# Performance work log

Hardware: AMD Instinct MI355X
Metric: run time of the kernel (lower is better)

Reference implementation:

```python
import jax, jax.numpy as jnp
import numpy as np

B, T1, T2, D = 4, 128, 128, 300


def setup_inputs() -> dict:
    key = jax.random.key(0)
    ks = jax.random.split(key, 9)
    s = 1.0 / np.sqrt(D)
    return {
        "query": jax.random.normal(ks[0], (B, T1, D), jnp.float32),
        "key": jax.random.normal(ks[1], (B, T2, D), jnp.float32),
        "value": jax.random.normal(ks[2], (B, T2, D), jnp.float32),
        "hL": jax.random.normal(ks[3], (B, T1, T2, D), jnp.float32),
        "hR": jax.random.normal(ks[4], (B, T2, T1, D), jnp.float32),
        "WQ": jax.random.uniform(ks[5], (D, D), jnp.float32, -s, s),
        "bQ": jax.random.uniform(ks[6], (D,), jnp.float32, -s, s),
        "WK": jax.random.uniform(ks[7], (D, D), jnp.float32, -s, s),
        "bK": jax.random.uniform(ks[8], (D,), jnp.float32, -s, s),
    }


def reference(query, key, value, hL, hR, WQ, bQ, WK, bK):
    # Linear projections (torch nn.Linear: x @ W.T + b). Note fwK is applied
    # to BOTH key and value in the original module.
    q = query @ WQ.T + bQ            # [B, T1, D]
    k = key @ WK.T + bK              # [B, T2, D]
    v = value @ WK.T + bK            # [B, T2, D]

    hR_t = jnp.swapaxes(hR, 1, 2)    # [B, T1, T2, D]

    # concept-augmented scores: (q_i + hL_ij) . (k_j + hR_ji)
    q_plus_hL = q[:, :, None, :] + hL          # [B, T1, T2, D]
    k_plus_hR = k[:, None, :, :] + hR_t        # [B, T1, T2, D]
    scores = jnp.einsum("bijd,bijd->bij", q_plus_hL, k_plus_hR)  # [B, T1, T2]

    p_attn = jax.nn.softmax(scores, axis=-1)   # [B, T1, T2] (dropout p=0.0)

    # sharpening=True path: re-softmax with temperature 1/1000 then clamp
    attn = jnp.clip(jax.nn.softmax(1000.0 * p_attn, axis=-1), 0.0, 1.0)

    v_aug = v[:, None, :, :] + hR_t            # [B, T1, T2, D]
    x = jnp.einsum("bij,bijd->bid", attn, v_aug)  # [B, T1, D]
    return x
```

## Files before the change

kernel.cpp:

```cpp
#include <hip/hip_runtime.h>

#define BB 4
#define T 128
#define D 300
#define D4 75
#define NROW 512

__global__ __launch_bounds__(320) void proj_kernel(
    const float* __restrict__ query, const float* __restrict__ key,
    const float* __restrict__ value,
    const float* __restrict__ WQ, const float* __restrict__ bQ,
    const float* __restrict__ WK, const float* __restrict__ bK,
    float* __restrict__ qkv )
{
    const int src  = blockIdx.x >> 6;
    const int rblk = blockIdx.x & 63;
    const int r0   = rblk * 8;
    const float* in   = (src == 0) ? query : (src == 1 ? key : value);
    const float* W    = (src == 0) ? WQ : WK;
    const float* bias = (src == 0) ? bQ : bK;
    float* out = qkv + src * (NROW * D);

    __shared__ __align__(16) float lds_in[8 * D];
    for (int idx = threadIdx.x; idx < 8 * D; idx += 320)
        lds_in[idx] = in[r0 * D + idx];
    __syncthreads();

    const int t = threadIdx.x;
    if (t < D) {
        float acc[8];
        const float bv = bias[t];
        #pragma unroll
        for (int r = 0; r < 8; ++r) acc[r] = bv;
        const float4* W4 = (const float4*)(W + t * D);
        for (int e4 = 0; e4 < D4; ++e4) {
            const float4 w = W4[e4];
            #pragma unroll
            for (int r = 0; r < 8; ++r) {
                const float4 x = *(const float4*)(&lds_in[r * D + e4 * 4]);
                acc[r] += w.x * x.x + w.y * x.y + w.z * x.z + w.w * x.w;
            }
        }
        #pragma unroll
        for (int r = 0; r < 8; ++r)
            out[(r0 + r) * D + t] = acc[r];
    }
}

__global__ __launch_bounds__(1024) void attn_kernel(
    const float* __restrict__ hL, const float* __restrict__ hR,
    const float* __restrict__ qkv, float* __restrict__ outp)
{
    const int b = blockIdx.x >> 7;
    const int i = blockIdx.x & 127;

    const float* qp    = qkv + (b * T + i) * D;
    const float* kbase = qkv + NROW * D + b * T * D;
    const float* vbase = qkv + 2 * NROW * D + b * T * D;

    __shared__ __align__(16) float q_lds[D];
    __shared__ float sc[T];
    __shared__ __align__(16) float red[12][D];

    for (int idx = threadIdx.x; idx < D; idx += 1024) q_lds[idx] = qp[idx];
    __syncthreads();

    const int wave = threadIdx.x >> 6;
    const int lane = threadIdx.x & 63;

    const float4* hL4 = (const float4*)(hL + (size_t)(b * T + i) * T * D);
    for (int j = wave; j < T; j += 16) {
        const float4* hRrow = (const float4*)(hR + ((size_t)(b * T + j) * T + i) * D);
        const float4* krow  = (const float4*)(kbase + j * D);
        float4 a = {0.f, 0.f, 0.f, 0.f};
        #pragma unroll
        for (int it = 0; it < 2; ++it) {
            const int d4 = lane + it * 64;
            if (d4 < D4) {
                const float4 l  = hL4[j * D4 + d4];
                const float4 r  = hRrow[d4];
                const float4 kk = krow[d4];
                const float4 qq = *(const float4*)(&q_lds[d4 * 4]);
                a.x += (qq.x + l.x) * (kk.x + r.x);
                a.y += (qq.y + l.y) * (kk.y + r.y);
                a.z += (qq.z + l.z) * (kk.z + r.z);
                a.w += (qq.w + l.w) * (kk.w + r.w);
            }
        }
        float s = a.x + a.y + a.z + a.w;
        #pragma unroll
        for (int off = 32; off > 0; off >>= 1)
            s += __shfl_down(s, off, 64);
        if (lane == 0) sc[j] = s;
    }
    __syncthreads();

    if (wave == 0) {
        float s0 = sc[lane], s1 = sc[lane + 64];
        float m = fmaxf(s0, s1);
        #pragma unroll
        for (int off = 32; off > 0; off >>= 1) m = fmaxf(m, __shfl_xor(m, off, 64));
        float e0 = __expf(s0 - m), e1 = __expf(s1 - m);
        float sum = e0 + e1;
        #pragma unroll
        for (int off = 32; off > 0; off >>= 1) sum += __shfl_xor(sum, off, 64);
        const float inv = 1.0f / sum;
        float t0 = 1000.0f * (e0 * inv), t1 = 1000.0f * (e1 * inv);
        float m2 = fmaxf(t0, t1);
        #pragma unroll
        for (int off = 32; off > 0; off >>= 1) m2 = fmaxf(m2, __shfl_xor(m2, off, 64));
        float f0 = __expf(t0 - m2), f1 = __expf(t1 - m2);
        float sum2 = f0 + f1;
        #pragma unroll
        for (int off = 32; off > 0; off >>= 1) sum2 += __shfl_xor(sum2, off, 64);
        const float inv2 = 1.0f / sum2;
        sc[lane]      = fminf(fmaxf(f0 * inv2, 0.f), 1.f);
        sc[lane + 64] = fminf(fmaxf(f1 * inv2, 0.f), 1.f);
    }
    __syncthreads();

    const int tid = threadIdx.x;
    if (tid < 12 * D4) {
        const int grp = tid / D4;
        const int d4  = tid % D4;
        float4 acc = {0.f, 0.f, 0.f, 0.f};
        for (int j = grp; j < T; j += 12) {
            const float aj = sc[j];
            if (aj >= 1e-12f) {
                const float4 v4 = *(const float4*)(vbase + j * D + d4 * 4);
                const float4 r4 = *(const float4*)(hR + ((size_t)(b * T + j) * T + i) * D + d4 * 4);
                acc.x += aj * (v4.x + r4.x);
                acc.y += aj * (v4.y + r4.y);
                acc.z += aj * (v4.z + r4.z);
                acc.w += aj * (v4.w + r4.w);
            }
        }
        *(float4*)(&red[grp][d4 * 4]) = acc;
    }
    __syncthreads();
    if (tid < D4) {
        float4 o = {0.f, 0.f, 0.f, 0.f};
        #pragma unroll
        for (int g = 0; g < 12; ++g) {
            const float4 p = *(const float4*)(&red[g][tid * 4]);
            o.x += p.x; o.y += p.y; o.z += p.z; o.w += p.w;
        }
        *(float4*)(outp + (size_t)(b * T + i) * D + tid * 4) = o;
    }
}

extern "C" void kernel_launch(void* const* d_in, const int* in_sizes, int n_in,
                              void* d_out, int out_size, void* d_ws, size_t ws_size,
                              hipStream_t stream) {
    const float* query = (const float*)d_in[0];
    const float* key   = (const float*)d_in[1];
    const float* value = (const float*)d_in[2];
    const float* hL    = (const float*)d_in[3];
    const float* hR    = (const float*)d_in[4];
    const float* WQ    = (const float*)d_in[5];
    const float* bQ    = (const float*)d_in[6];
    const float* WK    = (const float*)d_in[7];
    const float* bK    = (const float*)d_in[8];
    float* out = (float*)d_out;
    float* qkv = (float*)d_ws;

    proj_kernel<<<dim3(192), dim3(320), 0, stream>>>(query, key, value, WQ, bQ, WK, bK, qkv);
    attn_kernel<<<dim3(512), dim3(1024), 0, stream>>>(hL, hR, qkv, out);
}
```

Before: 227.4 us.

## Split attention into tiled score kernel and separate softmax/output kernel

Replaces the per-query-row attention kernel with a score kernel that processes 4x4 (i,j) tiles. Each tile stages contiguous 4-row runs of hL and hR into shared memory, so hR is read as contiguous chunks instead of one strided row per j. Scores go to a workspace buffer. A second kernel applies the double softmax and the weighted sum over v+hR with scalar loads per d. This adds a kernel launch and a round-trip of the scores through global memory, and hR is still read again with strides in the output phase.

```diff
diff --git a/kernel.cpp b/kernel.cpp
--- a/kernel.cpp
+++ b/kernel.cpp
@@ -47,56 +47,79 @@
     }
 }
 
-__global__ __launch_bounds__(1024) void attn_kernel(
+__global__ __launch_bounds__(256) void score_kernel(
     const float* __restrict__ hL, const float* __restrict__ hR,
-    const float* __restrict__ qkv, float* __restrict__ outp)
+    const float* __restrict__ qkv, float* __restrict__ S)
+{
+    const int b  = blockIdx.x >> 10;
+    const int it = (blockIdx.x >> 5) & 31;
+    const int jt = blockIdx.x & 31;
+    const int i0 = it * 4, j0 = jt * 4;
+
+    __shared__ __align__(16) float4 lds[2400];
+
+    const float4* hL4 = (const float4*)hL;
+    const float4* hR4 = (const float4*)hR;
+
+    for (int f = threadIdx.x; f < 2400; f += 256) {
+        if (f < 1200) {
+            const int run = f / 300;
+            const int t   = f - run * 300;
+            lds[f] = hL4[(size_t)((b * T + i0 + run) * T + j0) * D4 + t];
+        } else {
+            const int g   = f - 1200;
+            const int run = g / 300;
+            const int t   = g - run * 300;
+            lds[f] = hR4[(size_t)((b * T + j0 + run) * T + i0) * D4 + t];
+        }
+    }
+    __syncthreads();
+
+    const int w    = threadIdx.x >> 6;
+    const int lane = threadIdx.x & 63;
+
+    const float4* q4     = (const float4*)(qkv) + (size_t)(b * T + i0 + w) * D4;
+    const float4* kbase4 = (const float4*)(qkv + NROW * D);
+
+    const float4 qa = q4[lane];
+    float4 qb = {0.f, 0.f, 0.f, 0.f};
+    if (lane < D4 - 64) qb = q4[64 + lane];
+
+    #pragma unroll
+    for (int jl = 0; jl < 4; ++jl) {
+        const float4* k4 = kbase4 + (size_t)(b * T + j0 + jl) * D4;
+        const float4 ka = k4[lane];
+        const float4 la = lds[w * 300 + jl * 75 + lane];
+        const float4 ra = lds[1200 + jl * 300 + w * 75 + lane];
+        float s = (qa.x + la.x) * (ka.x + ra.x) + (qa.y + la.y) * (ka.y + ra.y)
+                + (qa.z + la.z) * (ka.z + ra.z) + (qa.w + la.w) * (ka.w + ra.w);
+        if (lane < D4 - 64) {
+            const float4 kb = k4[64 + lane];
+            const float4 lb = lds[w * 300 + jl * 75 + 64 + lane];
+            const float4 rb = lds[1200 + jl * 300 + w * 75 + 64 + lane];
+            s += (qb.x + lb.x) * (kb.x + rb.x) + (qb.y + lb.y) * (kb.y + rb.y)
+               + (qb.z + lb.z) * (kb.z + rb.z) + (qb.w + lb.w) * (kb.w + rb.w);
+        }
+        #pragma unroll
+        for (int off = 32; off > 0; off >>= 1)
+            s += __shfl_down(s, off, 64);
+        if (lane == 0)
+            S[(size_t)(b * T + i0 + w) * T + j0 + jl] = s;
+    }
+}
+
+__global__ __launch_bounds__(320) void out_kernel(
+    const float* __restrict__ S, const float* __restrict__ qkv,
+    const float* __restrict__ hR, float* __restrict__ outp)
 {
     const int b = blockIdx.x >> 7;
     const int i = blockIdx.x & 127;
+    __shared__ float sc[T];
+    const int tid = threadIdx.x;
 
-    const float* qp    = qkv + (b * T + i) * D;
-    const float* kbase = qkv + NROW * D + b * T * D;
-    const float* vbase = qkv + 2 * NROW * D + b * T * D;
-
-    __shared__ __align__(16) float q_lds[D];
-    __shared__ float sc[T];
-    __shared__ __align__(16) float red[12][D];
-
-    for (int idx = threadIdx.x; idx < D; idx += 1024) q_lds[idx] = qp[idx];
-    __syncthreads();
-
-    const int wave = threadIdx.x >> 6;
-    const int lane = threadIdx.x & 63;
-
-    const float4* hL4 = (const float4*)(hL + (size_t)(b * T + i) * T * D);
-    for (int j = wave; j < T; j += 16) {
-        const float4* hRrow = (const float4*)(hR + ((size_t)(b * T + j) * T + i) * D);
-        const float4* krow  = (const float4*)(kbase + j * D);
-        float4 a = {0.f, 0.f, 0.f, 0.f};
-        #pragma unroll
-        for (int it = 0; it < 2; ++it) {
-            const int d4 = lane + it * 64;
-            if (d4 < D4) {
-                const float4 l  = hL4[j * D4 + d4];
-                const float4 r  = hRrow[d4];
-                const float4 kk = krow[d4];
-                const float4 qq = *(const float4*)(&q_lds[d4 * 4]);
-                a.x += (qq.x + l.x) * (kk.x + r.x);
-                a.y += (qq.y + l.y) * (kk.y + r.y);
-                a.z += (qq.z + l.z) * (kk.z + r.z);
-                a.w += (qq.w + l.w) * (kk.w + r.w);
-            }
-        }
-        float s = a.x + a.y + a.z + a.w;
-        #pragma unroll
-        for (int off = 32; off > 0; off >>= 1)
-            s += __shfl_down(s, off, 64);
-        if (lane == 0) sc[j] = s;
-    }
-    __syncthreads();
-
-    if (wave == 0) {
-        float s0 = sc[lane], s1 = sc[lane + 64];
+    if (tid < 64) {
+        const float* Srow = S + (size_t)(b * T + i) * T;
+        float s0 = Srow[tid], s1 = Srow[tid + 64];
         float m = fmaxf(s0, s1);
         #pragma unroll
         for (int off = 32; off > 0; off >>= 1) m = fmaxf(m, __shfl_xor(m, off, 64));
@@ -114,38 +137,20 @@
         #pragma unroll
         for (int off = 32; off > 0; off >>= 1) sum2 += __shfl_xor(sum2, off, 64);
         const float inv2 = 1.0f / sum2;
-        sc[lane]      = fminf(fmaxf(f0 * inv2, 0.f), 1.f);
-        sc[lane + 64] = fminf(fmaxf(f1 * inv2, 0.f), 1.f);
+        sc[tid]      = fminf(fmaxf(f0 * inv2, 0.f), 1.f);
+        sc[tid + 64] = fminf(fmaxf(f1 * inv2, 0.f), 1.f);
     }
     __syncthreads();
 
-    const int tid = threadIdx.x;
-    if (tid < 12 * D4) {
-        const int grp = tid / D4;
-        const int d4  = tid % D4;
-        float4 acc = {0.f, 0.f, 0.f, 0.f};
-        for (int j = grp; j < T; j += 12) {
+    if (tid < D) {
+        float acc = 0.f;
+        const float* vb = qkv + 2 * NROW * D + b * T * D;
+        for (int j = 0; j < T; ++j) {
             const float aj = sc[j];
-            if (aj >= 1e-12f) {
-                const float4 v4 = *(const float4*)(vbase + j * D + d4 * 4);
-                const float4 r4 = *(const float4*)(hR + ((size_t)(b * T + j) * T + i) * D + d4 * 4);
-                acc.x += aj * (v4.x + r4.x);
-                acc.y += aj * (v4.y + r4.y);
-                acc.z += aj * (v4.z + r4.z);
-                acc.w += aj * (v4.w + r4.w);
-            }
+            if (aj >= 1e-12f)
+                acc += aj * (vb[j * D + tid] + hR[((size_t)(b * T + j) * T + i) * D + tid]);
         }
-        *(float4*)(&red[grp][d4 * 4]) = acc;
-    }
-    __syncthreads();
-    if (tid < D4) {
-        float4 o = {0.f, 0.f, 0.f, 0.f};
-        #pragma unroll
-        for (int g = 0; g < 12; ++g) {
-            const float4 p = *(const float4*)(&red[g][tid * 4]);
-            o.x += p.x; o.y += p.y; o.z += p.z; o.w += p.w;
-        }
-        *(float4*)(outp + (size_t)(b * T + i) * D + tid * 4) = o;
+        outp[(size_t)(b * T + i) * D + tid] = acc;
     }
 }
 
@@ -163,7 +168,9 @@
     const float* bK    = (const float*)d_in[8];
     float* out = (float*)d_out;
     float* qkv = (float*)d_ws;
+    float* S   = qkv + 3 * NROW * D;
 
     proj_kernel<<<dim3(192), dim3(320), 0, stream>>>(query, key, value, WQ, bQ, WK, bK, qkv);
-    attn_kernel<<<dim3(512), dim3(1024), 0, stream>>>(hL, hR, qkv, out);
+    score_kernel<<<dim3(4096), dim3(256), 0, stream>>>(hL, hR, qkv, S);
+    out_kernel<<<dim3(512), dim3(320), 0, stream>>>(S, qkv, hR, out);
 }
```

New measurement: 239.9 us. 1.05x slower.
